# Kernel optimization log

Hardware: AMD Instinct MI355X
Metric: run time of the kernel (lower is better)

Reference implementation:

```python
import jax, jax.numpy as jnp
import numpy as np

N = 60000   # cells
F = 256     # CELL_FEATURE_DIM
H = 128     # HIDDEN_DIM
NH = 8      # NUM_HEADS
DH = H // NH
L = 2       # NUM_LAYERS
C = 256     # tissue clusters
E = 600000  # cell edges
ET = 1500   # tissue edges
NCLS = 4


def _seg_softmax(s, seg, n):
    # numerically stable softmax within segments; s: [E, NH]
    m = jax.ops.segment_max(s, seg, num_segments=n)
    e = jnp.exp(s - m[seg])
    z = jax.ops.segment_sum(e, seg, num_segments=n)
    return e / z[seg]


def _forward(cell_features, cluster_labels, cell_edge_index, tissue_edge_index,
             W_cell_proj, b_cell_proj, W_tissue_proj, b_tissue_proj,
             gat_W, gat_asrc, gat_adst, gat_b, gcn_W, gcn_b,
             bu_Wq, bu_Wk, bu_Wv, bu_bq, bu_bk, bu_bv, bu_Wo, bu_bo,
             td_Wv, td_bv, td_Wo, td_bo,
             gru_Wih, gru_bih, gru_Whh, gru_bhh,
             Wc1, bc1, Wc2, bc2, Wc3, bc3):
    lab = cluster_labels
    # tissue node init = per-cluster mean of raw cell features (as in _construct_tissue_graph)
    cnt = jax.ops.segment_sum(jnp.ones((N,), jnp.float32), lab, num_segments=C)
    tissue_x = jax.ops.segment_sum(cell_features, lab, num_segments=C) / jnp.maximum(cnt, 1.0)[:, None]

    cell_h = cell_features @ W_cell_proj.T + b_cell_proj      # [N, H]
    tissue_h = tissue_x @ W_tissue_proj.T + b_tissue_proj     # [C, H]

    # add self-loops (PyG GATConv / GCNConv default)
    csrc = jnp.concatenate([cell_edge_index[0], jnp.arange(N, dtype=cell_edge_index.dtype)])
    cdst = jnp.concatenate([cell_edge_index[1], jnp.arange(N, dtype=cell_edge_index.dtype)])
    tsrc = jnp.concatenate([tissue_edge_index[0], jnp.arange(C, dtype=tissue_edge_index.dtype)])
    tdst = jnp.concatenate([tissue_edge_index[1], jnp.arange(C, dtype=tissue_edge_index.dtype)])

    # GCN symmetric norm (deg over col, PyG gcn_norm)
    degc = jax.ops.segment_sum(jnp.ones_like(tdst, dtype=jnp.float32), tdst, num_segments=C)
    dinv = jnp.where(degc > 0, 1.0 / jnp.sqrt(degc), 0.0)
    w_e = (dinv[tsrc] * dinv[tdst])[:, None]

    scale = 1.0 / jnp.sqrt(jnp.float32(DH))

    for l in range(L):
        # --- GATConv (multi-head concat) + ELU ---
        h = (cell_h @ gat_W[l].T).reshape(N, NH, DH)
        a_s = (h * gat_asrc[l]).sum(-1)  # [N, NH]
        a_d = (h * gat_adst[l]).sum(-1)
        e = jax.nn.leaky_relu(a_s[csrc] + a_d[cdst], negative_slope=0.2)  # [E+N, NH]
        alpha = _seg_softmax(e, cdst, N)
        agg = jax.ops.segment_sum(h[csrc] * alpha[:, :, None], cdst, num_segments=N)
        cell_h = jax.nn.elu(agg.reshape(N, H) + gat_b[l])

        # --- GCNConv + ReLU on tissue graph ---
        th = tissue_h @ gcn_W[l].T
        tissue_h = jax.nn.relu(jax.ops.segment_sum(th[tsrc] * w_e, tdst, num_segments=C) + gcn_b[l])

        # --- bottom-up cross-level attention: tissue queries attend over their cells ---
        q = ((tissue_h @ bu_Wq.T + bu_bq) * scale).reshape(C, NH, DH)
        k = (cell_h @ bu_Wk.T + bu_bk).reshape(N, NH, DH)
        v = (cell_h @ bu_Wv.T + bu_bv).reshape(N, NH, DH)
        s_att = (q[lab] * k).sum(-1)                       # [N, NH]
        al = _seg_softmax(s_att, lab, C)
        ctx = jax.ops.segment_sum(v * al[:, :, None], lab, num_segments=C).reshape(C, H)
        tissue_h = ctx @ bu_Wo.T + bu_bo

        # --- top-down attention: each cell attends to its single tissue node ---
        # softmax over one key is identically 1, so output = Wo(Wv t + bv) + bo gathered per cell
        td = (tissue_h @ td_Wv.T + td_bv) @ td_Wo.T + td_bo  # [C, H]
        cell_h = td[lab]

        # --- top-down GRUCell refinement: x=[cell;tissue], h=cell ---
        x_in = jnp.concatenate([cell_h, tissue_h[lab]], axis=-1)  # [N, 2H]
        gi = x_in @ gru_Wih.T + gru_bih
        gh = cell_h @ gru_Whh.T + gru_bhh
        r = jax.nn.sigmoid(gi[:, :H] + gh[:, :H])
        z = jax.nn.sigmoid(gi[:, H:2 * H] + gh[:, H:2 * H])
        n = jnp.tanh(gi[:, 2 * H:] + r * gh[:, 2 * H:])
        cell_h = (1.0 - z) * n + z * cell_h

    # dual-pooling readouts (single graph: batch all zeros)
    emb = jnp.concatenate([cell_h.mean(0), cell_h.max(0), tissue_h.mean(0), tissue_h.max(0)])[None, :]  # [1, 4H]
    h1 = jax.nn.relu(emb @ Wc1.T + bc1)
    h2 = jax.nn.relu(h1 @ Wc2.T + bc2)
    return h2 @ Wc3.T + bc3  # [1, NCLS]


def setup_inputs() -> dict:
    k = jax.random.split(jax.random.key(0), 40)
    s = 0.05
    r = lambda i, shape: jax.random.normal(k[i], shape, jnp.float32) * s
    return dict(
        cell_features=jax.random.normal(k[0], (N, F), jnp.float32),
        cell_edge_index=jax.random.randint(k[1], (2, E), 0, N),
        cluster_labels=jax.random.randint(k[2], (N,), 0, C),
        tissue_edge_index=jax.random.randint(k[3], (2, ET), 0, C),
        W_cell_proj=r(4, (H, F)), b_cell_proj=r(5, (H,)),
        W_tissue_proj=r(6, (H, F)), b_tissue_proj=r(7, (H,)),
        gat_W=r(8, (L, H, H)), gat_asrc=r(9, (L, NH, DH)), gat_adst=r(10, (L, NH, DH)), gat_b=r(11, (L, H)),
        gcn_W=r(12, (L, H, H)), gcn_b=r(13, (L, H)),
        bu_Wq=r(14, (H, H)), bu_Wk=r(15, (H, H)), bu_Wv=r(16, (H, H)),
        bu_bq=r(17, (H,)), bu_bk=r(18, (H,)), bu_bv=r(19, (H,)),
        bu_Wo=r(20, (H, H)), bu_bo=r(21, (H,)),
        td_Wv=r(22, (H, H)), td_bv=r(23, (H,)), td_Wo=r(24, (H, H)), td_bo=r(25, (H,)),
        gru_Wih=r(26, (3 * H, 2 * H)), gru_bih=r(27, (3 * H,)),
        gru_Whh=r(28, (3 * H, H)), gru_bhh=r(29, (3 * H,)),
        Wc1=r(30, (2 * H, 4 * H)), bc1=r(31, (2 * H,)),
        Wc2=r(32, (H, 2 * H)), bc2=r(33, (H,)),
        Wc3=r(34, (NCLS, H)), bc3=r(35, (NCLS,)),
    )


def reference(cell_features, cell_edge_index, cluster_labels, tissue_edge_index,
              W_cell_proj, b_cell_proj, W_tissue_proj, b_tissue_proj,
              gat_W, gat_asrc, gat_adst, gat_b, gcn_W, gcn_b,
              bu_Wq, bu_Wk, bu_Wv, bu_bq, bu_bk, bu_bv, bu_Wo, bu_bo,
              td_Wv, td_bv, td_Wo, td_bo,
              gru_Wih, gru_bih, gru_Whh, gru_bhh,
              Wc1, bc1, Wc2, bc2, Wc3, bc3):
    return _forward(cell_features, cluster_labels, cell_edge_index, tissue_edge_index,
                    W_cell_proj, b_cell_proj, W_tissue_proj, b_tissue_proj,
                    gat_W, gat_asrc, gat_adst, gat_b, gcn_W, gcn_b,
                    bu_Wq, bu_Wk, bu_Wv, bu_bq, bu_bk, bu_bv, bu_Wo, bu_bo,
                    td_Wv, td_bv, td_Wo, td_bo,
                    gru_Wih, gru_bih, gru_Whh, gru_bhh,
                    Wc1, bc1, Wc2, bc2, Wc3, bc3)
```

## Files before the change

kernel.cpp:

```cpp
#include <hip/hip_runtime.h>
#include <math.h>

constexpr int N  = 60000;
constexpr int F  = 256;
constexpr int H  = 128;
constexpr int C  = 256;
constexpr int E  = 600000;
constexpr int ET = 1500;
constexpr int NB = (N + 1023) / 1024;

__global__ void hg_hist(const int* __restrict__ cdst, int* __restrict__ deg,
                        const int* __restrict__ lab, int* __restrict__ ccnt) {
  int e = blockIdx.x * 256 + threadIdx.x;
  if (e < E) atomicAdd(&deg[cdst[e]], 1);
  if (e < N) atomicAdd(&ccnt[lab[e]], 1);
}

__global__ __launch_bounds__(256) void hg_scan1(const int* __restrict__ deg, int* __restrict__ off,
                                                int* __restrict__ btot, int n) {
  int b = blockIdx.x, t = threadIdx.x;
  int i0 = b * 1024 + t * 4;
  __shared__ int sums[256];
  int d0 = 0, d1 = 0, d2 = 0, d3 = 0;
  if (i0 + 3 < n) {
    int4 dd = *(const int4*)&deg[i0];
    d0 = dd.x; d1 = dd.y; d2 = dd.z; d3 = dd.w;
  } else {
    if (i0     < n) d0 = deg[i0];
    if (i0 + 1 < n) d1 = deg[i0 + 1];
    if (i0 + 2 < n) d2 = deg[i0 + 2];
    if (i0 + 3 < n) d3 = deg[i0 + 3];
  }
  int s = d0 + d1 + d2 + d3;
  sums[t] = s;
  __syncthreads();
  for (int ofs = 1; ofs < 256; ofs <<= 1) {
    int v = (t >= ofs) ? sums[t - ofs] : 0;
    __syncthreads();
    sums[t] += v;
    __syncthreads();
  }
  int excl = sums[t] - s;
  if (t == 255) btot[b] = sums[t];
  int run = excl;
  if (i0     < n) off[i0]     = run; run += d0;
  if (i0 + 1 < n) off[i0 + 1] = run; run += d1;
  if (i0 + 2 < n) off[i0 + 2] = run; run += d2;
  if (i0 + 3 < n) off[i0 + 3] = run;
}

__global__ __launch_bounds__(256) void hg_scan2_setup(int* __restrict__ btot, int* __restrict__ off,
                                                      const int* __restrict__ ccnt, int* __restrict__ coff,
                                                      const int* __restrict__ tsrc, const int* __restrict__ tdst,
                                                      int* __restrict__ toff, int* __restrict__ tlist,
                                                      float* __restrict__ dinv) {
  __shared__ int sa[256], sb[256], sc2[256];
  int t = threadIdx.x;
  if (blockIdx.x == 0) {
    if (t < 64) sa[t] = (t < NB) ? btot[t] : 0;
    __syncthreads();
    if (t == 0) {
      int r = 0;
      for (int i = 0; i < NB; ++i) { int v = sa[i]; sa[i] = r; r += v; }
      off[N] = r;
    }
    __syncthreads();
    if (t < NB) btot[t] = sa[t];
  } else if (blockIdx.x == 1) {
    int v0 = ccnt[t];
    sa[t] = v0;
    __syncthreads();
    for (int ofs = 1; ofs < 256; ofs <<= 1) {
      int v = (t >= ofs) ? sa[t - ofs] : 0;
      __syncthreads();
      sa[t] += v;
      __syncthreads();
    }
    coff[t + 1] = sa[t];
    if (t == 0) coff[0] = 0;
  } else {
    sa[t] = 0;
    __syncthreads();
    for (int e = t; e < ET; e += 256) atomicAdd(&sa[tdst[e]], 1);
    __syncthreads();
    int v = sa[t];
    dinv[t] = rsqrtf((float)(v + 1));
    sb[t] = v;
    __syncthreads();
    for (int ofs = 1; ofs < 256; ofs <<= 1) {
      int u = (t >= ofs) ? sb[t - ofs] : 0;
      __syncthreads();
      sb[t] += u;
      __syncthreads();
    }
    toff[t + 1] = sb[t];
    if (t == 0) toff[0] = 0;
    sc2[t] = sb[t] - v;
    __syncthreads();
    for (int e = t; e < ET; e += 256) {
      int d = tdst[e];
      int p = atomicAdd(&sc2[d], 1);
      tlist[p] = tsrc[e];
    }
  }
}

__global__ void hg_scan3(int* __restrict__ off, const int* __restrict__ btot, int n) {
  int b = blockIdx.x;
  int addv = btot[b];
  int i0 = b * 1024 + threadIdx.x * 4;
#pragma unroll
  for (int r = 0; r < 4; ++r)
    if (i0 + r < n) off[i0 + r] += addv;
}

__global__ void hg_scatter(const int* __restrict__ csrc, const int* __restrict__ cdst,
                           const int* __restrict__ off, int* __restrict__ cur, int* __restrict__ csr,
                           const int* __restrict__ lab, const int* __restrict__ coff,
                           int* __restrict__ ccur, int* __restrict__ list) {
  int e = blockIdx.x * 256 + threadIdx.x;
  if (e < E) {
    int d = cdst[e];
    int p = atomicAdd(&cur[d], 1);
    csr[off[d] + p] = csrc[e];
  }
  if (e < N) {
    int c = lab[e];
    int p = atomicAdd(&ccur[c], 1);
    list[coff[c] + p] = e;
  }
}

struct TJob { const float* src; float* dst; int SR; int SC; int dld; };
struct PrepArgs {
  TJob j[8];
  const float* gatW1; const float* Wcp; const float* bcp; float* Wcompt; float* bcomp;
  const float* tdWo; const float* tdWv; const float* tdbv; const float* tdbo;
  float* A_td; float* Wcat_t; float* bcat;
};

__global__ __launch_bounds__(256) void hg_prep1(PrepArgs a) {
  int y = blockIdx.y, t = threadIdx.x;
  if (y < 8) {
    TJob jb = a.j[y];
    int total = jb.SR * jb.SC;
    for (int idx = blockIdx.x * 256 + t; idx < total; idx += gridDim.x * 256) {
      int r = idx / jb.SC, c = idx - r * jb.SC;
      jb.dst[(size_t)c * jb.dld + r] = jb.src[idx];
    }
  } else if (y == 8) {
    int j = blockIdx.x, k = t;
    float acc = 0.f;
#pragma unroll 4
    for (int m = 0; m < 128; ++m) acc = fmaf(a.gatW1[j * 128 + m], a.Wcp[m * 256 + k], acc);
    a.Wcompt[k * 128 + j] = acc;
    if (k == 0) {
      float b = 0.f;
      for (int m = 0; m < 128; ++m) b = fmaf(a.gatW1[j * 128 + m], a.bcp[m], b);
      a.bcomp[j] = b;
    }
  } else if (blockIdx.x < 64) {
    int j = blockIdx.x * 2 + (t >> 7), k = t & 127;
    float acc = 0.f;
#pragma unroll 4
    for (int p = 0; p < 128; ++p) acc = fmaf(a.tdWo[j * 128 + p], a.tdWv[p * 128 + k], acc);
    a.A_td[j * 128 + k] = acc;
    a.Wcat_t[k * 896 + j] = acc;
    if (k == 0) {
      float b = 0.f;
      for (int p = 0; p < 128; ++p) b = fmaf(a.tdWo[j * 128 + p], a.tdbv[p], b);
      a.bcat[j] = b + a.tdbo[j];
    }
  }
}

__global__ __launch_bounds__(256) void hg_pc2b(const float* __restrict__ Wih, const float* __restrict__ bih,
                                               const float* __restrict__ Whh, const float* __restrict__ bhh,
                                               const float* __restrict__ A_td, float* __restrict__ Wcat_t,
                                               float* __restrict__ bcat) {
  int jj = blockIdx.x * 2 + (threadIdx.x >> 7), k = threadIdx.x & 127;
  const float* coef;
  float extra, bb;
  int dcol, j;
  if (jj < 384) {
    j = jj; coef = Wih + (size_t)j * 256; extra = Wih[(size_t)j * 256 + 128 + k]; dcol = 128 + j; bb = bih[j];
  } else {
    j = jj - 384; coef = Whh + (size_t)j * 128; extra = 0.f; dcol = 512 + j; bb = bhh[j];
  }
  float a = 0.f;
#pragma unroll 4
  for (int m = 0; m < 128; ++m) a = fmaf(coef[m], A_td[m * 128 + k], a);
  Wcat_t[k * 896 + dcol] = a + extra;
  if (k == 0) {
    float b = 0.f;
    for (int m = 0; m < 128; ++m) b = fmaf(coef[m], bcat[m], b);
    bcat[dcol] = b + bb;
  }
}

__global__ __launch_bounds__(256, 3) void hg_gemm_coef(
    const float* __restrict__ A, int M, int rtiles,
    const float* __restrict__ Wt, const float* __restrict__ bias,
    float* __restrict__ outp,
    const float* __restrict__ avs, const float* __restrict__ avd,
    float* __restrict__ o_s, float* __restrict__ o_d,
    const int* __restrict__ list, const int* __restrict__ coff,
    const float* __restrict__ Wtpt, const float* __restrict__ btp, float* __restrict__ tish) {
  __shared__ float Al[32][132];
  __shared__ float Wl[32][132];
  const int t = threadIdx.x;

  if (blockIdx.x >= rtiles) {
    int c = blockIdx.x - rtiles;
    float* mrow = (float*)Al;
    int s0 = coff[c], n = coff[c + 1] - s0;
    float acc = 0.f;
#pragma unroll 4
    for (int i = 0; i < n; ++i) acc += A[(size_t)list[s0 + i] * F + t];
    mrow[t] = acc / fmaxf((float)n, 1.f);
    __syncthreads();
    if (t < 128) {
      float a = btp[t];
#pragma unroll 4
      for (int k = 0; k < 256; ++k) a = fmaf(mrow[k], Wtpt[k * 128 + t], a);
      tish[c * 128 + t] = a;
    }
    return;
  }

  const int tx = t & 15, ty = t >> 4;
  const int m0 = blockIdx.x * 128;

  float acc[8][8];
#pragma unroll
  for (int r = 0; r < 8; ++r)
#pragma unroll
    for (int c = 0; c < 8; ++c) acc[r][c] = 0.f;

  const int arow = t & 127, akh = t >> 7;
  const int wkr = t >> 3, wc0 = (t & 7) * 4;
  const int agm = m0 + arow;

  for (int kc = 0; kc < 256; kc += 32) {
#pragma unroll
    for (int f = 0; f < 4; ++f) {
      int k_off = akh * 16 + f * 4;
      float4 a = make_float4(0.f, 0.f, 0.f, 0.f);
      if (agm < M) a = *(const float4*)&A[(size_t)agm * 256 + kc + k_off];
      Al[k_off][arow] = a.x;
      Al[k_off + 1][arow] = a.y;
      Al[k_off + 2][arow] = a.z;
      Al[k_off + 3][arow] = a.w;
    }
#pragma unroll
    for (int f = 0; f < 4; ++f) {
      *(float4*)&Wl[wkr][wc0 + f * 32] = *(const float4*)&Wt[(size_t)(kc + wkr) * 128 + wc0 + f * 32];
    }
    __syncthreads();
#pragma unroll 2
    for (int kk = 0; kk < 32; ++kk) {
      float4 a0 = *(const float4*)&Al[kk][ty * 4];
      float4 a1 = *(const float4*)&Al[kk][64 + ty * 4];
      float4 w0 = *(const float4*)&Wl[kk][tx * 4];
      float4 w1 = *(const float4*)&Wl[kk][64 + tx * 4];
      float ar[8] = {a0.x, a0.y, a0.z, a0.w, a1.x, a1.y, a1.z, a1.w};
      float wr[8] = {w0.x, w0.y, w0.z, w0.w, w1.x, w1.y, w1.z, w1.w};
#pragma unroll
      for (int r = 0; r < 8; ++r)
#pragma unroll
        for (int c = 0; c < 8; ++c) acc[r][c] = fmaf(ar[r], wr[c], acc[r][c]);
    }
    __syncthreads();
  }

  {
    float bA[8];
#pragma unroll
    for (int c = 0; c < 4; ++c) {
      bA[c] = bias[tx * 4 + c];
      bA[4 + c] = bias[64 + tx * 4 + c];
    }
#pragma unroll
    for (int r = 0; r < 8; ++r)
#pragma unroll
      for (int c = 0; c < 8; ++c) acc[r][c] += bA[c];
  }

#pragma unroll
  for (int r = 0; r < 8; ++r) {
    int gm = m0 + ((r < 4) ? (ty * 4 + r) : (64 + ty * 4 + r - 4));
    if (gm < M) {
      float* op = outp + (size_t)gm * 128 + tx * 4;
      *(float4*)op        = make_float4(acc[r][0], acc[r][1], acc[r][2], acc[r][3]);
      *(float4*)(op + 64) = make_float4(acc[r][4], acc[r][5], acc[r][6], acc[r][7]);
    }
  }

  {
    float4 s0 = *(const float4*)&avs[tx * 4], s1 = *(const float4*)&avs[64 + tx * 4];
    float4 d0 = *(const float4*)&avd[tx * 4], d1 = *(const float4*)&avd[64 + tx * 4];
#pragma unroll
    for (int r = 0; r < 8; ++r) {
      int gm = m0 + ((r < 4) ? (ty * 4 + r) : (64 + ty * 4 + r - 4));
      float psA = acc[r][0] * s0.x + acc[r][1] * s0.y + acc[r][2] * s0.z + acc[r][3] * s0.w;
      float psB = acc[r][4] * s1.x + acc[r][5] * s1.y + acc[r][6] * s1.z + acc[r][7] * s1.w;
      float pdA = acc[r][0] * d0.x + acc[r][1] * d0.y + acc[r][2] * d0.z + acc[r][3] * d0.w;
      float pdB = acc[r][4] * d1.x + acc[r][5] * d1.y + acc[r][6] * d1.z + acc[r][7] * d1.w;
      psA += __shfl_xor(psA, 1); psA += __shfl_xor(psA, 2);
      psB += __shfl_xor(psB, 1); psB += __shfl_xor(psB, 2);
      pdA += __shfl_xor(pdA, 1); pdA += __shfl_xor(pdA, 2);
      pdB += __shfl_xor(pdB, 1); pdB += __shfl_xor(pdB, 2);
      if ((tx & 3) == 0 && gm < M) {
        int h = tx >> 2;
        o_s[(size_t)gm * 8 + h] = psA;
        o_s[(size_t)gm * 8 + 4 + h] = psB;
        o_d[(size_t)gm * 8 + h] = pdA;
        o_d[(size_t)gm * 8 + 4 + h] = pdB;
      }
    }
  }
}

#define GMAXE 64
__global__ __launch_bounds__(256) void hg_gat_agg(
    const float* __restrict__ hproj, const float* __restrict__ a_s,
    const float* __restrict__ a_d, const int* __restrict__ remap,
    const int* __restrict__ off, const int* __restrict__ csr,
    const float* __restrict__ bias, float* __restrict__ outh,
    const float* __restrict__ qk, const float* __restrict__ qb,
    const int* __restrict__ lab, const int* __restrict__ nodelist,
    float* __restrict__ satt, int nNodes) {
  const int wid = threadIdx.x >> 6;
  const int l = threadIdx.x & 63;
  const int gid = blockIdx.x * 4 + wid;
  __shared__ int srcs_s[4][GMAXE];
  __shared__ float w_s[4][GMAXE][8];
  if (gid >= nNodes) return;
  const int node = nodelist[gid];
  int* srcs = srcs_s[wid];
  float (*wls)[8] = w_s[wid];
  const int o0 = off[node], deg = off[node + 1] - o0;
  const int cl = lab[node];
  const int dl = remap ? cl : node;
  const int hsc = l & 7;
  const int q4 = l & 31;
  const int sub = l >> 5;
  const int hq = q4 >> 2;
  const float adh = a_d[dl * 8 + hsc];
  const float ash = a_s[dl * 8 + hsc];
  float msc = -INFINITY, zsc = 0.f;
  float4 acc = make_float4(0.f, 0.f, 0.f, 0.f);
  const float4* hp4 = (const float4*)hproj;

  for (int cb = 0; cb < deg; cb += GMAXE) {
    const int len = min(GMAXE, deg - cb);
    if (l < len) {
      int s = csr[o0 + cb + l];
      srcs[l] = remap ? remap[s] : s;
    }
    asm volatile("s_waitcnt lgkmcnt(0)" ::: "memory");
    float lm = -INFINITY;
    for (int base = 0; base < len; base += 8) {
      int e = base + (l >> 3);
      if (e < len) {
        float sc = a_s[srcs[e] * 8 + hsc] + adh;
        sc = sc > 0.f ? sc : 0.2f * sc;
        wls[e][hsc] = sc;
        lm = fmaxf(lm, sc);
      }
    }
    lm = fmaxf(lm, __shfl_xor(lm, 8));
    lm = fmaxf(lm, __shfl_xor(lm, 16));
    lm = fmaxf(lm, __shfl_xor(lm, 32));
    float mnew = fmaxf(msc, lm);
    float rs = __expf(msc - mnew);
    float zc = 0.f;
    asm volatile("s_waitcnt lgkmcnt(0)" ::: "memory");
    for (int base = 0; base < len; base += 8) {
      int e = base + (l >> 3);
      if (e < len) {
        float wv = __expf(wls[e][hsc] - mnew);
        wls[e][hsc] = wv;
        zc += wv;
      }
    }
    asm volatile("s_waitcnt lgkmcnt(0)" ::: "memory");
    zc += __shfl_xor(zc, 8); zc += __shfl_xor(zc, 16); zc += __shfl_xor(zc, 32);
    zsc = zsc * rs + zc;
    msc = mnew;
    float rsa = __shfl(rs, hq);
    acc.x *= rsa; acc.y *= rsa; acc.z *= rsa; acc.w *= rsa;
    for (int e = sub; e < len; e += 2) {
      float wv = wls[e][hq];
      float4 hv = hp4[(size_t)srcs[e] * 32 + q4];
      acc.x = fmaf(wv, hv.x, acc.x);
      acc.y = fmaf(wv, hv.y, acc.y);
      acc.z = fmaf(wv, hv.z, acc.z);
      acc.w = fmaf(wv, hv.w, acc.w);
    }
  }
  float ssl = ash + adh;
  ssl = ssl > 0.f ? ssl : 0.2f * ssl;
  float mnew = fmaxf(msc, ssl);
  float rs = __expf(msc - mnew);
  float wsl = __expf(ssl - mnew);
  zsc = zsc * rs + wsl;
  float rsa = __shfl(rs, hq);
  float wsa = __shfl(wsl, hq);
  float zh = __shfl(zsc, hq);
  acc.x *= rsa; acc.y *= rsa; acc.z *= rsa; acc.w *= rsa;
  acc.x += __shfl_xor(acc.x, 32);
  acc.y += __shfl_xor(acc.y, 32);
  acc.z += __shfl_xor(acc.z, 32);
  acc.w += __shfl_xor(acc.w, 32);
  float4 hv = hp4[(size_t)dl * 32 + q4];
  acc.x = fmaf(wsa, hv.x, acc.x);
  acc.y = fmaf(wsa, hv.y, acc.y);
  acc.z = fmaf(wsa, hv.z, acc.z);
  acc.w = fmaf(wsa, hv.w, acc.w);
  float inv = 1.f / zh;
  float4 bv4 = *(const float4*)&bias[q4 * 4];
  float4 o;
  o.x = acc.x * inv + bv4.x;
  o.y = acc.y * inv + bv4.y;
  o.z = acc.z * inv + bv4.z;
  o.w = acc.w * inv + bv4.w;
  o.x = o.x > 0.f ? o.x : __expf(o.x) - 1.f;
  o.y = o.y > 0.f ? o.y : __expf(o.y) - 1.f;
  o.z = o.z > 0.f ? o.z : __expf(o.z) - 1.f;
  o.w = o.w > 0.f ? o.w : __expf(o.w) - 1.f;
  if (sub == 0) ((float4*)outh)[(size_t)node * 32 + q4] = o;

  const float4* qk4 = (const float4*)(qk + (size_t)cl * 1024);
  float p0, p1, p2, p3;
  {
    float4 qv0 = qk4[(sub * 4 + 0) * 32 + q4];
    float4 qv1 = qk4[(sub * 4 + 1) * 32 + q4];
    float4 qv2 = qk4[(sub * 4 + 2) * 32 + q4];
    float4 qv3 = qk4[(sub * 4 + 3) * 32 + q4];
    p0 = o.x * qv0.x + o.y * qv0.y + o.z * qv0.z + o.w * qv0.w;
    p1 = o.x * qv1.x + o.y * qv1.y + o.z * qv1.z + o.w * qv1.w;
    p2 = o.x * qv2.x + o.y * qv2.y + o.z * qv2.z + o.w * qv2.w;
    p3 = o.x * qv3.x + o.y * qv3.y + o.z * qv3.z + o.w * qv3.w;
  }
  int b4f = (l >> 4) & 1, b3f = (l >> 3) & 1;
  float snd0 = b4f ? p0 : p2, snd1 = b4f ? p1 : p3;
  float kp0  = b4f ? p2 : p0, kp1  = b4f ? p3 : p1;
  kp0 += __shfl_xor(snd0, 16);
  kp1 += __shfl_xor(snd1, 16);
  float snd = b3f ? kp0 : kp1;
  float kp  = b3f ? kp1 : kp0;
  kp += __shfl_xor(snd, 8);
  kp += __shfl_xor(kp, 4);
  kp += __shfl_xor(kp, 2);
  kp += __shfl_xor(kp, 1);
  int h = sub * 4 + b4f * 2 + b3f;
  if ((l & 7) == 0) satt[(size_t)node * 8 + h] = kp + qb[cl * 8 + h];
}

__global__ __launch_bounds__(128) void hg_gcn_q(const float* __restrict__ tin, const int* __restrict__ toff,
                                                const int* __restrict__ tlist, const float* __restrict__ dinv,
                                                const float* __restrict__ gt, const float* __restrict__ gcnb,
                                                const float* __restrict__ Wqt, const float* __restrict__ bq,
                                                const float* __restrict__ Wk, const float* __restrict__ bk,
                                                float* __restrict__ qk, float* __restrict__ qb) {
  int c = blockIdx.x, t = threadIdx.x;
  __shared__ float xa[128], trow[128], qrow[128];
  float dc = dinv[c];
  float acc = tin[c * 128 + t] * dc * dc;
  int s0 = toff[c], s1 = toff[c + 1];
  for (int i = s0; i < s1; ++i) {
    int s = tlist[i];
    acc = fmaf(tin[s * 128 + t], dinv[s] * dc, acc);
  }
  xa[t] = acc;
  __syncthreads();
  float th = 0.f;
#pragma unroll 4
  for (int k = 0; k < 128; ++k) th = fmaf(xa[k], gt[k * 128 + t], th);
  float vv = fmaxf(th + gcnb[t], 0.f);
  trow[t] = vv;
  __syncthreads();
  float qa = bq[t];
#pragma unroll 4
  for (int k = 0; k < 128; ++k) qa = fmaf(trow[k], Wqt[k * 128 + t], qa);
  qrow[t] = qa * 0.25f;
  __syncthreads();
#pragma unroll
  for (int h = 0; h < 8; ++h) {
    float s = 0.f;
#pragma unroll
    for (int j = 0; j < 16; ++j) s = fmaf(Wk[(size_t)(h * 16 + j) * 128 + t], qrow[h * 16 + j], s);
    qk[((size_t)c * 8 + h) * 128 + t] = s;
  }
  if (t < 8) {
    float s = 0.f;
#pragma unroll
    for (int j = 0; j < 16; ++j) s = fmaf(qrow[t * 16 + j], bk[t * 16 + j], s);
    qb[c * 8 + t] = s;
  }
}

__global__ __launch_bounds__(256) void hg_bu_chain(
    const float* __restrict__ s_att, const float* __restrict__ hcell,
    const int* __restrict__ list, const int* __restrict__ coff,
    const float* __restrict__ Wv, const float* __restrict__ bv,
    const float* __restrict__ Wot, const float* __restrict__ bo,
    const float* __restrict__ Wcat_t, const float* __restrict__ bcat,
    const float* __restrict__ gatWt, const float* __restrict__ avs, const float* __restrict__ avd,
    float* __restrict__ tish, float* __restrict__ ccell,
    float* __restrict__ hprojc, float* __restrict__ a_s2, float* __restrict__ a_d2) {
  int c = blockIdx.x, t = threadIdx.x;
  int s0 = coff[c], n = coff[c + 1] - s0;
  int tf = t & 127, half = t >> 7;
  __shared__ float red[32][8];
  __shared__ float mh[8], zh[8];
  __shared__ int cells[64];
  __shared__ float wl[64][8];
  __shared__ float msh[8][128];
  __shared__ float b0[128], b1[128], part[2][128], catv[896];
  int g = t >> 3, h8 = t & 7;
  float lm = -INFINITY;
  for (int i = g; i < n; i += 32) lm = fmaxf(lm, s_att[(size_t)list[s0 + i] * 8 + h8]);
  red[g][h8] = lm;
  __syncthreads();
  if (t < 8) {
    float m2 = -INFINITY;
#pragma unroll
    for (int i = 0; i < 32; ++i) m2 = fmaxf(m2, red[i][t]);
    mh[t] = m2;
  }
  __syncthreads();
  const float mloc = mh[t & 7];
  float zp = 0.f;
  float macc[8] = {0.f, 0.f, 0.f, 0.f, 0.f, 0.f, 0.f, 0.f};
  for (int cb = 0; cb < n; cb += 64) {
    int len = min(64, n - cb);
    if (t < len) cells[t] = list[s0 + cb + t];
    __syncthreads();
#pragma unroll
    for (int p = 0; p < 2; ++p) {
      int e = p * 32 + (t >> 3);
      if (e < len) {
        float w = __expf(s_att[(size_t)cells[e] * 8 + (t & 7)] - mloc);
        wl[e][t & 7] = w;
        zp += w;
      }
    }
    __syncthreads();
    for (int e = half; e < len; e += 2) {
      float x = hcell[(size_t)cells[e] * 128 + tf];
      float4 w0 = *(const float4*)&wl[e][0];
      float4 w1 = *(const float4*)&wl[e][4];
      macc[0] = fmaf(w0.x, x, macc[0]);
      macc[1] = fmaf(w0.y, x, macc[1]);
      macc[2] = fmaf(w0.z, x, macc[2]);
      macc[3] = fmaf(w0.w, x, macc[3]);
      macc[4] = fmaf(w1.x, x, macc[4]);
      macc[5] = fmaf(w1.y, x, macc[5]);
      macc[6] = fmaf(w1.z, x, macc[6]);
      macc[7] = fmaf(w1.w, x, macc[7]);
    }
    __syncthreads();
  }
  red[t >> 3][t & 7] = zp;
  __syncthreads();
  if (t < 8) {
    float z = 0.f;
#pragma unroll
    for (int i = 0; i < 32; ++i) z += red[i][t];
    zh[t] = (n > 0) ? 1.f / z : 0.f;
  }
  if (half) {
#pragma unroll
    for (int h = 0; h < 8; ++h) msh[h][tf] = macc[h];
  }
  __syncthreads();
  if (!half) {
#pragma unroll
    for (int h = 0; h < 8; ++h) msh[h][tf] = (macc[h] + msh[h][tf]) * zh[h];
  }
  __syncthreads();
  {
    int h = tf >> 4;
    float ps = 0.f;
    const float* wp = Wv + (size_t)tf * 128 + half * 64;
    const float* mp = &msh[h][half * 64];
#pragma unroll 4
    for (int k = 0; k < 64; ++k) ps = fmaf(wp[k], mp[k], ps);
    part[half][tf] = ps;
  }
  __syncthreads();
  if (t < 128) b0[t] = part[0][t] + part[1][t] + bv[t];
  __syncthreads();
  int ks = half;
  {
    float ps = 0.f;
    const float* wp = Wot + (size_t)ks * 64 * 128 + tf;
#pragma unroll 4
    for (int k = 0; k < 64; ++k) ps = fmaf(b0[ks * 64 + k], wp[k * 128], ps);
    part[ks][tf] = ps;
  }
  __syncthreads();
  if (t < 128) {
    float vv = part[0][t] + part[1][t] + bo[t];
    b1[t] = vv;
    tish[c * 128 + t] = vv;
  }
  __syncthreads();
  for (int j = t; j < 896; j += 256) {
    float a = bcat[j];
#pragma unroll 4
    for (int k = 0; k < 128; ++k) a = fmaf(b1[k], Wcat_t[k * 896 + j], a);
    catv[j] = a;
  }
  __syncthreads();
  if (t < 128) {
    float td = catv[t];
    float r = 1.f / (1.f + expf(-(catv[128 + t] + catv[512 + t])));
    float zz = 1.f / (1.f + expf(-(catv[256 + t] + catv[640 + t])));
    float nn = tanhf(catv[384 + t] + r * catv[768 + t]);
    float cn = (1.f - zz) * nn + zz * td;
    ccell[c * 128 + t] = cn;
    b0[t] = cn;
  }
  __syncthreads();
  if (gatWt) {
    float ps = 0.f;
    const float* wp = gatWt + (size_t)ks * 64 * 128 + tf;
#pragma unroll 4
    for (int k = 0; k < 64; ++k) ps = fmaf(b0[ks * 64 + k], wp[k * 128], ps);
    part[ks][tf] = ps;
    __syncthreads();
    if (t < 128) {
      float hp = part[0][t] + part[1][t];
      hprojc[c * 128 + t] = hp;
      float pss = hp * avs[t], pdd = hp * avd[t];
      pss += __shfl_xor(pss, 1); pss += __shfl_xor(pss, 2); pss += __shfl_xor(pss, 4); pss += __shfl_xor(pss, 8);
      pdd += __shfl_xor(pdd, 1); pdd += __shfl_xor(pdd, 2); pdd += __shfl_xor(pdd, 4); pdd += __shfl_xor(pdd, 8);
      if ((t & 15) == 0) {
        a_s2[c * 8 + (t >> 4)] = pss;
        a_d2[c * 8 + (t >> 4)] = pdd;
      }
    }
  }
}

__global__ __launch_bounds__(256) void hg_readout(const float* __restrict__ ccell2, const float* __restrict__ tish,
                                                  const int* __restrict__ cnt, const float* __restrict__ Wc1t,
                                                  const float* __restrict__ bc1, const float* __restrict__ Wc2t,
                                                  const float* __restrict__ bc2, const float* __restrict__ Wc3,
                                                  const float* __restrict__ bc3, float* __restrict__ outp) {
  __shared__ float emb[512], h1s[256], h2s[128];
  int t = threadIdx.x;
  if (t < 128) {
    float sm = 0.f, mx = -INFINITY;
    for (int c = 0; c < C; ++c) {
      float vv = ccell2[c * 128 + t];
      int n = cnt[c];
      sm += (float)n * vv;
      if (n > 0) mx = fmaxf(mx, vv);
    }
    emb[t] = sm / (float)N;
    emb[128 + t] = mx;
  } else {
    int tt = t - 128;
    float sm = 0.f, mx = -INFINITY;
    for (int c = 0; c < C; ++c) {
      float vv = tish[c * 128 + tt];
      sm += vv;
      mx = fmaxf(mx, vv);
    }
    emb[256 + tt] = sm * (1.f / (float)C);
    emb[384 + tt] = mx;
  }
  __syncthreads();
  float a = bc1[t];
#pragma unroll 4
  for (int kk = 0; kk < 512; ++kk) a = fmaf(emb[kk], Wc1t[kk * 256 + t], a);
  h1s[t] = fmaxf(a, 0.f);
  __syncthreads();
  if (t < 128) {
    float a2 = bc2[t];
#pragma unroll 4
    for (int kk = 0; kk < 256; ++kk) a2 = fmaf(h1s[kk], Wc2t[kk * 128 + t], a2);
    h2s[t] = fmaxf(a2, 0.f);
  }
  __syncthreads();
  if (t < 4) {
    float o = bc3[t];
    for (int kk = 0; kk < 128; ++kk) o = fmaf(h2s[kk], Wc3[t * 128 + kk], o);
    outp[t] = o;
  }
}

extern "C" void kernel_launch(void* const* d_in, const int* in_sizes, int n_in,
                              void* d_out, int out_size, void* d_ws, size_t ws_size,
                              hipStream_t stream) {
  (void)in_sizes; (void)n_in; (void)out_size; (void)ws_size;
  const float* feat  = (const float*)d_in[0];
  const int*   eidx  = (const int*)d_in[1];
  const int*   lab   = (const int*)d_in[2];
  const int*   tidx  = (const int*)d_in[3];
  const float* Wcp   = (const float*)d_in[4];
  const float* bcp   = (const float*)d_in[5];
  const float* Wtp   = (const float*)d_in[6];
  const float* btp   = (const float*)d_in[7];
  const float* gatW  = (const float*)d_in[8];
  const float* gasrc = (const float*)d_in[9];
  const float* gadst = (const float*)d_in[10];
  const float* gatb  = (const float*)d_in[11];
  const float* gcnW  = (const float*)d_in[12];
  const float* gcnb  = (const float*)d_in[13];
  const float* buWq  = (const float*)d_in[14];
  const float* buWk  = (const float*)d_in[15];
  const float* buWv  = (const float*)d_in[16];
  const float* bubq  = (const float*)d_in[17];
  const float* bubk  = (const float*)d_in[18];
  const float* bubv  = (const float*)d_in[19];
  const float* buWo  = (const float*)d_in[20];
  const float* bubo  = (const float*)d_in[21];
  const float* tdWv  = (const float*)d_in[22];
  const float* tdbv  = (const float*)d_in[23];
  const float* tdWo  = (const float*)d_in[24];
  const float* tdbo  = (const float*)d_in[25];
  const float* Wih   = (const float*)d_in[26];
  const float* bih   = (const float*)d_in[27];
  const float* Whh   = (const float*)d_in[28];
  const float* bhh   = (const float*)d_in[29];
  const float* Wc1   = (const float*)d_in[30];
  const float* bc1   = (const float*)d_in[31];
  const float* Wc2   = (const float*)d_in[32];
  const float* bc2   = (const float*)d_in[33];
  const float* Wc3   = (const float*)d_in[34];
  const float* bc3   = (const float*)d_in[35];
  float* outp = (float*)d_out;

  const int* csrc = eidx;
  const int* cdst = eidx + E;
  const int* tsrc = tidx;
  const int* tdst = tidx + ET;

  char* w = (char*)d_ws;
  auto alloc = [&](size_t bytes) -> void* {
    void* p = (void*)w;
    w += (bytes + 255) & ~(size_t)255;
    return p;
  };
  char* cnt0 = w;
  int* deg_cell = (int*)alloc((size_t)N * 4);
  int* cur_cell = (int*)alloc((size_t)N * 4);
  int* clu_cnt  = (int*)alloc((size_t)C * 4);
  int* clu_cur  = (int*)alloc((size_t)C * 4);
  size_t cntBytes = (size_t)(w - cnt0);
  int* off_cell = (int*)alloc((size_t)(N + 1) * 4);
  int* btot     = (int*)alloc(64 * 4);
  int* csr      = (int*)alloc((size_t)E * 4);
  int* clu_off  = (int*)alloc((size_t)(C + 1) * 4);
  int* clu_list = (int*)alloc((size_t)N * 4);
  int* toff     = (int*)alloc((size_t)(C + 1) * 4);
  int* tlist    = (int*)alloc((size_t)ET * 4);
  float* dinv   = (float*)alloc((size_t)C * 4);
  float* buf1   = (float*)alloc((size_t)N * 128 * 4);
  float* buf2   = (float*)alloc((size_t)N * 128 * 4);
  float* a_s    = (float*)alloc((size_t)N * 8 * 4);
  float* a_d    = (float*)alloc((size_t)N * 8 * 4);
  float* s_att  = (float*)alloc((size_t)N * 8 * 4);
  float* tish   = (float*)alloc((size_t)C * 128 * 4);
  float* qkb    = (float*)alloc((size_t)C * 8 * 128 * 4);
  float* qbb    = (float*)alloc((size_t)C * 8 * 4);
  float* ccell  = (float*)alloc((size_t)C * 128 * 4);
  float* hprojc = (float*)alloc((size_t)C * 128 * 4);
  float* a_sc   = (float*)alloc((size_t)C * 8 * 4);
  float* a_dc   = (float*)alloc((size_t)C * 8 * 4);
  float* A_td   = (float*)alloc(128 * 128 * 4);
  float* Wcat_t = (float*)alloc(128 * 896 * 4);
  float* bcat   = (float*)alloc(896 * 4);
  float* Wcompt = (float*)alloc(256 * 128 * 4);
  float* bcomp  = (float*)alloc(128 * 4);
  float* Wtpt   = (float*)alloc(256 * 128 * 4);
  float* g1t    = (float*)alloc(128 * 128 * 4);
  float* g2t    = (float*)alloc(128 * 128 * 4);
  float* Wqt    = (float*)alloc(128 * 128 * 4);
  float* Wot    = (float*)alloc(128 * 128 * 4);
  float* gatW2t = (float*)alloc(128 * 128 * 4);
  float* Wc1t   = (float*)alloc(512 * 256 * 4);
  float* Wc2t   = (float*)alloc(256 * 128 * 4);

  hipMemsetAsync(cnt0, 0, cntBytes, stream);

  hg_hist<<<(E + 255) / 256, 256, 0, stream>>>(cdst, deg_cell, lab, clu_cnt);
  hg_scan1<<<NB, 256, 0, stream>>>(deg_cell, off_cell, btot, N);
  hg_scan2_setup<<<3, 256, 0, stream>>>(btot, off_cell, clu_cnt, clu_off, tsrc, tdst, toff, tlist, dinv);
  hg_scan3<<<NB, 256, 0, stream>>>(off_cell, btot, N);
  hg_scatter<<<(E + 255) / 256, 256, 0, stream>>>(csrc, cdst, off_cell, cur_cell, csr,
                                                  lab, clu_off, clu_cur, clu_list);

  PrepArgs pa;
  pa.j[0] = {Wtp,            Wtpt,   128, 256, 128};
  pa.j[1] = {gcnW,           g1t,    128, 128, 128};
  pa.j[2] = {gcnW + 128*128, g2t,    128, 128, 128};
  pa.j[3] = {buWq,           Wqt,    128, 128, 128};
  pa.j[4] = {buWo,           Wot,    128, 128, 128};
  pa.j[5] = {gatW + 128*128, gatW2t, 128, 128, 128};
  pa.j[6] = {Wc1,            Wc1t,   256, 512, 256};
  pa.j[7] = {Wc2,            Wc2t,   128, 256, 128};
  pa.gatW1 = gatW; pa.Wcp = Wcp; pa.bcp = bcp; pa.Wcompt = Wcompt; pa.bcomp = bcomp;
  pa.tdWo = tdWo; pa.tdWv = tdWv; pa.tdbv = tdbv; pa.tdbo = tdbo;
  pa.A_td = A_td; pa.Wcat_t = Wcat_t; pa.bcat = bcat;
  hg_prep1<<<dim3(128, 10), 256, 0, stream>>>(pa);
  hg_pc2b<<<384, 256, 0, stream>>>(Wih, bih, Whh, bhh, A_td, Wcat_t, bcat);

  const int RT = (N + 127) / 128;
  hg_gemm_coef<<<RT + C, 256, 0, stream>>>(feat, N, RT, Wcompt, bcomp, buf2, gasrc, gadst, a_s, a_d,
                                           clu_list, clu_off, Wtpt, btp, tish);
  hg_gcn_q<<<C, 128, 0, stream>>>(tish, toff, tlist, dinv, g1t, gcnb, Wqt, bubq, buWk, bubk, qkb, qbb);
  hg_gat_agg<<<(N + 3) / 4, 256, 0, stream>>>(buf2, a_s, a_d, nullptr, off_cell, csr, gatb, buf1,
                                              qkb, qbb, lab, clu_list, s_att, N);
  hg_bu_chain<<<C, 256, 0, stream>>>(s_att, buf1, clu_list, clu_off, buWv, bubv, Wot, bubo, Wcat_t, bcat,
                                     gatW2t, gasrc + 128, gadst + 128, tish, ccell, hprojc, a_sc, a_dc);
  hg_gcn_q<<<C, 128, 0, stream>>>(tish, toff, tlist, dinv, g2t, gcnb + 128, Wqt, bubq, buWk, bubk, qkb, qbb);
  hg_gat_agg<<<(N + 3) / 4, 256, 0, stream>>>(hprojc, a_sc, a_dc, lab, off_cell, csr, gatb + 128, buf1,
                                              qkb, qbb, lab, clu_list, s_att, N);
  hg_bu_chain<<<C, 256, 0, stream>>>(s_att, buf1, clu_list, clu_off, buWv, bubv, Wot, bubo, Wcat_t, bcat,
                                     nullptr, nullptr, nullptr, tish, ccell, nullptr, nullptr, nullptr);

  hg_readout<<<1, 256, 0, stream>>>(ccell, tish, clu_cnt, Wc1t, bc1, Wc2t, bc2, Wc3, bc3, outp);
}
```

Baseline: 615.6 us.

## Split per-cluster bottom-up attention into parallel partial softmax blocks plus merge

The bottom-up cluster attention previously ran one block per cluster (256 blocks), each walking all of a cluster's cells serially. It now splits each cluster's cell list into 8 chunks processed by separate blocks. Each block writes a partial max, partial sum and weighted accumulator, and the chain kernel merges them flash-softmax style before the projection chain. This raises parallelism on the GPU's many CUs, at the cost of an extra launch and partial-buffer traffic of about 8 MB per layer.

Measured after the change: 570.3 us. 1.08x faster.

```diff
diff --git a/kernel.cpp b/kernel.cpp
--- a/kernel.cpp
+++ b/kernel.cpp
@@ -8,6 +8,7 @@
 constexpr int E  = 600000;
 constexpr int ET = 1500;
 constexpr int NB = (N + 1023) / 1024;
+constexpr int SPL = 8;
 
 __global__ void hg_hist(const int* __restrict__ cdst, int* __restrict__ deg,
                         const int* __restrict__ lab, int* __restrict__ ccnt) {
@@ -501,27 +502,24 @@
   }
 }
 
-__global__ __launch_bounds__(256) void hg_bu_chain(
+__global__ __launch_bounds__(256) void hg_bu_part(
     const float* __restrict__ s_att, const float* __restrict__ hcell,
     const int* __restrict__ list, const int* __restrict__ coff,
-    const float* __restrict__ Wv, const float* __restrict__ bv,
-    const float* __restrict__ Wot, const float* __restrict__ bo,
-    const float* __restrict__ Wcat_t, const float* __restrict__ bcat,
-    const float* __restrict__ gatWt, const float* __restrict__ avs, const float* __restrict__ avd,
-    float* __restrict__ tish, float* __restrict__ ccell,
-    float* __restrict__ hprojc, float* __restrict__ a_s2, float* __restrict__ a_d2) {
-  int c = blockIdx.x, t = threadIdx.x;
+    float* __restrict__ pm, float* __restrict__ pz, float* __restrict__ pmacc) {
+  int c = blockIdx.x, sp = blockIdx.y, t = threadIdx.x;
   int s0 = coff[c], n = coff[c + 1] - s0;
+  int chunk = (n + SPL - 1) / SPL;
+  int b0 = min(n, sp * chunk), b1 = min(n, b0 + chunk);
+  int cnt = b1 - b0;
   int tf = t & 127, half = t >> 7;
   __shared__ float red[32][8];
-  __shared__ float mh[8], zh[8];
+  __shared__ float mh[8];
   __shared__ int cells[64];
   __shared__ float wl[64][8];
   __shared__ float msh[8][128];
-  __shared__ float b0[128], b1[128], part[2][128], catv[896];
   int g = t >> 3, h8 = t & 7;
   float lm = -INFINITY;
-  for (int i = g; i < n; i += 32) lm = fmaxf(lm, s_att[(size_t)list[s0 + i] * 8 + h8]);
+  for (int i = g; i < cnt; i += 32) lm = fmaxf(lm, s_att[(size_t)list[s0 + b0 + i] * 8 + h8]);
   red[g][h8] = lm;
   __syncthreads();
   if (t < 8) {
@@ -534,9 +532,9 @@
   const float mloc = mh[t & 7];
   float zp = 0.f;
   float macc[8] = {0.f, 0.f, 0.f, 0.f, 0.f, 0.f, 0.f, 0.f};
-  for (int cb = 0; cb < n; cb += 64) {
-    int len = min(64, n - cb);
-    if (t < len) cells[t] = list[s0 + cb + t];
+  for (int cb = 0; cb < cnt; cb += 64) {
+    int len = min(64, cnt - cb);
+    if (t < len) cells[t] = list[s0 + b0 + cb + t];
     __syncthreads();
 #pragma unroll
     for (int p = 0; p < 2; ++p) {
@@ -565,11 +563,13 @@
   }
   red[t >> 3][t & 7] = zp;
   __syncthreads();
+  int pidx = (c * SPL + sp) * 8;
   if (t < 8) {
     float z = 0.f;
 #pragma unroll
     for (int i = 0; i < 32; ++i) z += red[i][t];
-    zh[t] = (n > 0) ? 1.f / z : 0.f;
+    pz[pidx + t] = z;
+    pm[pidx + t] = mh[t];
   }
   if (half) {
 #pragma unroll
@@ -578,7 +578,53 @@
   __syncthreads();
   if (!half) {
 #pragma unroll
-    for (int h = 0; h < 8; ++h) msh[h][tf] = (macc[h] + msh[h][tf]) * zh[h];
+    for (int h = 0; h < 8; ++h) pmacc[(size_t)(pidx + h) * 128 + tf] = macc[h] + msh[h][tf];
+  }
+}
+
+__global__ __launch_bounds__(256) void hg_bu_chain(
+    const float* __restrict__ pm, const float* __restrict__ pz, const float* __restrict__ pmacc,
+    const float* __restrict__ Wv, const float* __restrict__ bv,
+    const float* __restrict__ Wot, const float* __restrict__ bo,
+    const float* __restrict__ Wcat_t, const float* __restrict__ bcat,
+    const float* __restrict__ gatWt, const float* __restrict__ avs, const float* __restrict__ avd,
+    float* __restrict__ tish, float* __restrict__ ccell,
+    float* __restrict__ hprojc, float* __restrict__ a_s2, float* __restrict__ a_d2) {
+  int c = blockIdx.x, t = threadIdx.x;
+  int tf = t & 127, half = t >> 7;
+  __shared__ float mh[8], zh[8];
+  __shared__ float sscale[SPL][8];
+  __shared__ float msh[8][128];
+  __shared__ float b0[128], b1[128], part[2][128], catv[896];
+  const int pbase = c * SPL * 8;
+  if (t < 8) {
+    float mg = -INFINITY;
+#pragma unroll
+    for (int s = 0; s < SPL; ++s) mg = fmaxf(mg, pm[pbase + s * 8 + t]);
+    mh[t] = mg;
+  }
+  __syncthreads();
+  if (t < SPL * 8) {
+    int s = t >> 3, h = t & 7;
+    float ms = pm[pbase + s * 8 + h];
+    sscale[s][h] = (ms > -1e37f) ? __expf(ms - mh[h]) : 0.f;
+  }
+  __syncthreads();
+  if (t < 8) {
+    float z = 0.f;
+#pragma unroll
+    for (int s = 0; s < SPL; ++s) z += pz[pbase + s * 8 + t] * sscale[s][t];
+    zh[t] = (z > 0.f) ? 1.f / z : 0.f;
+  }
+  __syncthreads();
+#pragma unroll
+  for (int hh = 0; hh < 4; ++hh) {
+    int h = half * 4 + hh;
+    float a = 0.f;
+#pragma unroll
+    for (int s = 0; s < SPL; ++s)
+      a = fmaf(pmacc[(size_t)(pbase + s * 8 + h) * 128 + tf], sscale[s][h], a);
+    msh[h][tf] = a * zh[h];
   }
   __syncthreads();
   {
@@ -773,6 +819,9 @@
   float* hprojc = (float*)alloc((size_t)C * 128 * 4);
   float* a_sc   = (float*)alloc((size_t)C * 8 * 4);
   float* a_dc   = (float*)alloc((size_t)C * 8 * 4);
+  float* pm     = (float*)alloc((size_t)C * SPL * 8 * 4);
+  float* pz     = (float*)alloc((size_t)C * SPL * 8 * 4);
+  float* pmacc  = (float*)alloc((size_t)C * SPL * 8 * 128 * 4);
   float* A_td   = (float*)alloc(128 * 128 * 4);
   float* Wcat_t = (float*)alloc(128 * 896 * 4);
   float* bcat   = (float*)alloc(896 * 4);
@@ -817,12 +866,14 @@
   hg_gcn_q<<<C, 128, 0, stream>>>(tish, toff, tlist, dinv, g1t, gcnb, Wqt, bubq, buWk, bubk, qkb, qbb);
   hg_gat_agg<<<(N + 3) / 4, 256, 0, stream>>>(buf2, a_s, a_d, nullptr, off_cell, csr, gatb, buf1,
                                               qkb, qbb, lab, clu_list, s_att, N);
-  hg_bu_chain<<<C, 256, 0, stream>>>(s_att, buf1, clu_list, clu_off, buWv, bubv, Wot, bubo, Wcat_t, bcat,
+  hg_bu_part<<<dim3(C, SPL), 256, 0, stream>>>(s_att, buf1, clu_list, clu_off, pm, pz, pmacc);
+  hg_bu_chain<<<C, 256, 0, stream>>>(pm, pz, pmacc, buWv, bubv, Wot, bubo, Wcat_t, bcat,
                                      gatW2t, gasrc + 128, gadst + 128, tish, ccell, hprojc, a_sc, a_dc);
   hg_gcn_q<<<C, 128, 0, stream>>>(tish, toff, tlist, dinv, g2t, gcnb + 128, Wqt, bubq, buWk, bubk, qkb, qbb);
   hg_gat_agg<<<(N + 3) / 4, 256, 0, stream>>>(hprojc, a_sc, a_dc, lab, off_cell, csr, gatb + 128, buf1,
                                               qkb, qbb, lab, clu_list, s_att, N);
-  hg_bu_chain<<<C, 256, 0, stream>>>(s_att, buf1, clu_list, clu_off, buWv, bubv, Wot, bubo, Wcat_t, bcat,
+  hg_bu_part<<<dim3(C, SPL), 256, 0, stream>>>(s_att, buf1, clu_list, clu_off, pm, pz, pmacc);
+  hg_bu_chain<<<C, 256, 0, stream>>>(pm, pz, pmacc, buWv, bubv, Wot, bubo, Wcat_t, bcat,
                                      nullptr, nullptr, nullptr, tish, ccell, nullptr, nullptr, nullptr);
 
   hg_readout<<<1, 256, 0, stream>>>(ccell, tish, clu_cnt, Wc1t, bc1, Wc2t, bc2, Wc3, bc3, outp);
```
